# Optimization experiments

Hardware: AMD Instinct MI355X
Metric: run time of the kernel (lower is better)

## Reference

```python
import jax, jax.numpy as jnp
import numpy as np

E = 8           # num_experts
K = 2           # num_experts_per_tok
D = 1024        # hidden_size
F = 2048        # intermediate_dim
B, S = 1, 2048  # batch, seq_len


def setup_inputs() -> dict:
    key = jax.random.key(0)
    k0, k1, k2, k3, k4, k5 = jax.random.split(key, 6)
    hidden_states = jax.random.normal(k0, (B, S, D), dtype=jnp.float32)
    topk_weights = jax.random.uniform(k1, (B * S, K), dtype=jnp.float32)
    topk_ids = jax.random.randint(k2, (B * S, K), 0, E, dtype=jnp.int32)
    scale = 0.02
    wi_0 = jax.random.normal(k3, (E, D, F), dtype=jnp.float32) * scale
    wi_1 = jax.random.normal(k4, (E, D, F), dtype=jnp.float32) * scale
    wo = jax.random.normal(k5, (E, F, D), dtype=jnp.float32) * scale
    return {"hidden_states": hidden_states, "topk_weights": topk_weights,
            "topk_ids": topk_ids, "wi_0": wi_0, "wi_1": wi_1, "wo": wo}


def _gmm(x, w, group_sizes):
    """Grouped matmul: rows of x are sorted by expert; group_sizes[e] rows use w[e].
    Small fixed loop over experts (E=8); rows not owned by expert e are masked out."""
    n_e = w.shape[0]
    expert_of_row = jnp.repeat(jnp.arange(n_e), group_sizes,
                               total_repeat_length=x.shape[0])  # [M]
    out = jnp.zeros((x.shape[0], w.shape[2]), dtype=x.dtype)
    for e in range(n_e):
        out = out + jnp.where((expert_of_row == e)[:, None], x @ w[e], 0.0)
    return out


def _moe_forward(hidden_states, topk_weights, topk_ids, wi_0, wi_1, wo):
    b, s, d = hidden_states.shape
    k = topk_ids.shape[1]
    n_e = wi_0.shape[0]
    x2d = hidden_states.reshape(b * s, d)

    # ---- permute: sort expanded tokens by selected expert (stable) ----
    flat_experts = jnp.ravel(topk_ids)                       # [T*K]
    sort_idx = jnp.argsort(flat_experts, stable=True)        # [T*K]
    sorted_rows = sort_idx // k                              # source token per row
    x_sorted = jnp.take(x2d, sorted_rows, axis=0)            # [T*K, D]
    group_sizes = jnp.bincount(flat_experts, length=n_e)     # [E]

    # ---- grouped GEMMs with SwiGLU (gate * up, then down) ----
    g0 = _gmm(x_sorted, wi_0, group_sizes)                   # [T*K, F]
    g1 = _gmm(x_sorted, wi_1, group_sizes)                   # [T*K, F]
    h = jax.nn.silu(g0) * g1                                 # fused SiLU-gate
    y = _gmm(h, wo, group_sizes)                             # [T*K, D]

    # ---- unpermute and combine with routing weights (fp32 accum) ----
    unsort_idx = jnp.argsort(sort_idx, stable=True)
    y = jnp.take(y, unsort_idx, axis=0).reshape(b * s, k, d)
    out = jnp.einsum('bke,bk->be', y.astype(jnp.float32),
                     topk_weights.astype(jnp.float32))
    return out.reshape(b, s, d)


def reference(hidden_states, topk_weights, topk_ids, wi_0, wi_1, wo):
    return _moe_forward(hidden_states, topk_weights, topk_ids, wi_0, wi_1, wo)
```

## Files before the change

kernel.cpp:

```cpp
#include <hip/hip_runtime.h>
#include <hip/hip_bf16.h>


#define D_DIM 1024
#define F_DIM 2048
#define ROWS 4096
#define MAXTILE 40
#define LDK 72

using f32x4 = __attribute__((ext_vector_type(4))) float;
using s16x8 = __attribute__((ext_vector_type(8))) short;

__device__ __forceinline__ unsigned pack_trunc(float lo, float hi) {
  return (__float_as_uint(lo) >> 16) | (__float_as_uint(hi) & 0xffff0000u);
}
__device__ __forceinline__ unsigned short bf_rn(float f) {
  unsigned u = __float_as_uint(f);
  u += 0x7fffu + ((u >> 16) & 1u);
  return (unsigned short)(u >> 16);
}
__device__ __forceinline__ unsigned pack_rn(float lo, float hi) {
  return (unsigned)bf_rn(lo) | ((unsigned)bf_rn(hi) << 16);
}

typedef const __attribute__((address_space(1))) void* gp_t;
typedef __attribute__((address_space(3))) void* lp_t;
__device__ __forceinline__ void load16(const void* g, void* l) {
  __builtin_amdgcn_global_load_lds((gp_t)g, (lp_t)l, 16, 0, 0);
}

__global__ __launch_bounds__(512) void route_kernel(const int* __restrict__ ids,
                                                    int* __restrict__ sorted_flat,
                                                    int* __restrict__ unsort,
                                                    int* __restrict__ tile_meta) {
  __shared__ int cnt[8];
  __shared__ int off[9];
  const int tid = threadIdx.x;
  const int w = tid >> 6, lane = tid & 63;
  int c = 0;
  for (int base = 0; base < ROWS; base += 64) {
    int e = ids[base + lane];
    c += __popcll(__ballot(e == w));
  }
  if (lane == 0) cnt[w] = c;
  __syncthreads();
  if (tid == 0) {
    int o = 0;
    for (int e = 0; e < 8; e++) { off[e] = o; o += cnt[e]; }
    off[8] = o;
    int nT = 0;
    for (int e = 0; e < 8; e++) {
      for (int r0 = off[e]; r0 < off[e + 1]; r0 += 128) {
        tile_meta[1 + 3 * nT] = r0;
        tile_meta[2 + 3 * nT] = off[e + 1];
        tile_meta[3 + 3 * nT] = e;
        nT++;
      }
    }
    tile_meta[0] = nT;
  }
  __syncthreads();
  int pos = off[w];
  const unsigned long long below = (1ull << lane) - 1ull;
  for (int base = 0; base < ROWS; base += 64) {
    int e = ids[base + lane];
    unsigned long long m = __ballot(e == w);
    if (e == w) {
      int p = pos + __popcll(m & below);
      sorted_flat[p] = base + lane;
      unsort[base + lane] = p;
    }
    pos += __popcll(m);
  }
}

__global__ void zero_kernel(float4* __restrict__ p, int n4) {
  int i = blockIdx.x * blockDim.x + threadIdx.x;
  if (i < n4) p[i] = float4{0.f, 0.f, 0.f, 0.f};
}

__global__ __launch_bounds__(256) void convT_lds(
    const float* __restrict__ wi0, const float* __restrict__ wi1,
    const float* __restrict__ wo, unsigned short* __restrict__ w0T,
    unsigned short* __restrict__ w1T, unsigned short* __restrict__ woT) {
  __shared__ unsigned t[64 * 33];
  const int z = blockIdx.y;
  const int which = z >> 3, e = z & 7;
  const float* S;
  unsigned short* Dp;
  int Kd, Nd, nbits;
  if (which == 0)      { S = wi0; Dp = w0T; Kd = D_DIM; Nd = F_DIM; nbits = 5; }
  else if (which == 1) { S = wi1; Dp = w1T; Kd = D_DIM; Nd = F_DIM; nbits = 5; }
  else                 { S = wo;  Dp = woT; Kd = F_DIM; Nd = D_DIM; nbits = 4; }
  S  += (size_t)e * Kd * Nd;
  Dp += (size_t)e * Kd * Nd;
  const int n0 = (blockIdx.x & ((1 << nbits) - 1)) * 64;
  const int k0 = (blockIdx.x >> nbits) * 64;
  const int tid = threadIdx.x;
  const int nb = (tid & 15) * 4;
#pragma unroll
  for (int i = 0; i < 2; i++) {
    const int kp = (tid >> 4) + i * 16;
    const float* p = S + (size_t)(k0 + 2 * kp) * Nd + n0 + nb;
    float4 v0 = *(const float4*)p;
    float4 v1 = *(const float4*)(p + Nd);
    t[(nb + 0) * 33 + kp] = pack_rn(v0.x, v1.x);
    t[(nb + 1) * 33 + kp] = pack_rn(v0.y, v1.y);
    t[(nb + 2) * 33 + kp] = pack_rn(v0.z, v1.z);
    t[(nb + 3) * 33 + kp] = pack_rn(v0.w, v1.w);
  }
  __syncthreads();
  const int co = (tid & 7) * 4;
#pragma unroll
  for (int i = 0; i < 2; i++) {
    const int n = (tid >> 3) + i * 32;
    const unsigned* q = &t[n * 33 + co];
    uint4 o = make_uint4(q[0], q[1], q[2], q[3]);
    *(uint4*)(Dp + (size_t)(n0 + n) * Kd + k0 + co * 2) = o;
  }
}

__global__ __launch_bounds__(256) void gather_kernel(const float* __restrict__ x,
                                                     const int* __restrict__ sorted_flat,
                                                     unsigned short* __restrict__ xs) {
  const int r = blockIdx.x;
  const int tok = sorted_flat[r] >> 1;
  const float4 v = *(const float4*)(x + (size_t)tok * D_DIM + threadIdx.x * 4);
  *(uint2*)(xs + (size_t)r * D_DIM + threadIdx.x * 4) =
      make_uint2(pack_rn(v.x, v.y), pack_rn(v.z, v.w));
}

__device__ __forceinline__ int sw(int row, int chunk) {
  return row * 64 + ((chunk ^ (row & 7)) << 3);
}

__global__ __launch_bounds__(256, 2) void gemm1_kernel(
    const unsigned short* __restrict__ xs, const unsigned short* __restrict__ w0T,
    const unsigned short* __restrict__ w1T, const int* __restrict__ tile_meta,
    unsigned short* __restrict__ h) {
  __shared__ unsigned short As[128 * 64];
  __shared__ unsigned short B0s[128 * 64];
  __shared__ unsigned short B1s[128 * 64];
  const int tile = blockIdx.x;
  if (tile >= tile_meta[0]) return;
  const int row0 = tile_meta[1 + 3 * tile];
  const int rowEnd = tile_meta[2 + 3 * tile];
  const int e = tile_meta[3 + 3 * tile];
  const int n0 = blockIdx.y * 128;
  const unsigned short* W0 = w0T + ((size_t)e * F_DIM + n0) * D_DIM;
  const unsigned short* W1 = w1T + ((size_t)e * F_DIM + n0) * D_DIM;

  const int tid = threadIdx.x;
  const int lane = tid & 63, wv = tid >> 6;
  const int wm = (wv & 1) * 64, wn = (wv >> 1) * 64;
  const int lm = lane & 15, lq = lane >> 4;
  const int srow = lane >> 3;
  const int skk = ((lane & 7) ^ srow) << 3;

  f32x4 acc0[4][4], acc1[4][4];
#pragma unroll
  for (int i = 0; i < 4; i++)
#pragma unroll
    for (int j = 0; j < 4; j++) { acc0[i][j] = 0.f; acc1[i][j] = 0.f; }

  for (int k0 = 0; k0 < D_DIM; k0 += 64) {
    __syncthreads();
#pragma unroll
    for (int r = 0; r < 4; r++) {
      const int c = r * 4 + wv;
      const int m = c * 8 + srow;
      int mc = row0 + m; if (mc > ROWS - 1) mc = ROWS - 1;
      load16(xs + (size_t)mc * D_DIM + k0 + skk, (char*)As + c * 1024);
      load16(W0 + (size_t)m * D_DIM + k0 + skk, (char*)B0s + c * 1024);
      load16(W1 + (size_t)m * D_DIM + k0 + skk, (char*)B1s + c * 1024);
    }
    __syncthreads();
#pragma unroll
    for (int ks = 0; ks < 64; ks += 32) {
      const int cb = (ks >> 3) + lq;
      s16x8 af[4], b0[4], b1[4];
#pragma unroll
      for (int t = 0; t < 4; t++) {
        af[t] = *(const s16x8*)&As[sw(wm + t * 16 + lm, cb)];
        b0[t] = *(const s16x8*)&B0s[sw(wn + t * 16 + lm, cb)];
        b1[t] = *(const s16x8*)&B1s[sw(wn + t * 16 + lm, cb)];
      }
#pragma unroll
      for (int im = 0; im < 4; im++)
#pragma unroll
        for (int in = 0; in < 4; in++) {
          acc0[im][in] = __builtin_amdgcn_mfma_f32_16x16x32_bf16(
              af[im], b0[in], acc0[im][in], 0, 0, 0);
          acc1[im][in] = __builtin_amdgcn_mfma_f32_16x16x32_bf16(
              af[im], b1[in], acc1[im][in], 0, 0, 0);
        }
    }
  }
#pragma unroll
  for (int im = 0; im < 4; im++) {
    int gmB = row0 + wm + im * 16 + lq * 4;
#pragma unroll
    for (int in = 0; in < 4; in++) {
      int gn = n0 + wn + in * 16 + lm;
#pragma unroll
      for (int r = 0; r < 4; r++) {
        int gm = gmB + r;
        if (gm < rowEnd) {
          float g = acc0[im][in][r];
          float s = g / (1.f + __expf(-g));
          h[(size_t)gm * F_DIM + gn] = bf_rn(s * acc1[im][in][r]);
        }
      }
    }
  }
}

__global__ __launch_bounds__(256, 4) void gemm2_kernel(
    const unsigned short* __restrict__ h, const unsigned short* __restrict__ woT,
    const int* __restrict__ tile_meta, float* __restrict__ y) {
  __shared__ unsigned short As[128 * 64];
  __shared__ unsigned short Bs[64 * 64];
  const int tile = blockIdx.x;
  if (tile >= tile_meta[0]) return;
  const int row0 = tile_meta[1 + 3 * tile];
  const int rowEnd = tile_meta[2 + 3 * tile];
  const int e = tile_meta[3 + 3 * tile];
  const int n0 = blockIdx.y * 64;
  const unsigned short* W = woT + ((size_t)e * D_DIM + n0) * F_DIM;

  const int tid = threadIdx.x;
  const int lane = tid & 63, wv = tid >> 6;
  const int wm = (wv & 1) * 64, wn = (wv >> 1) * 32;
  const int lm = lane & 15, lq = lane >> 4;
  const int srow = lane >> 3;
  const int skk = ((lane & 7) ^ srow) << 3;

  f32x4 acc[4][2];
#pragma unroll
  for (int i = 0; i < 4; i++)
#pragma unroll
    for (int j = 0; j < 2; j++) acc[i][j] = 0.f;

  for (int k0 = 0; k0 < F_DIM; k0 += 64) {
    __syncthreads();
#pragma unroll
    for (int r = 0; r < 4; r++) {
      const int c = r * 4 + wv;
      const int m = c * 8 + srow;
      int mc = row0 + m; if (mc > ROWS - 1) mc = ROWS - 1;
      load16(h + (size_t)mc * F_DIM + k0 + skk, (char*)As + c * 1024);
    }
#pragma unroll
    for (int r = 0; r < 2; r++) {
      const int c = r * 4 + wv;
      const int m = c * 8 + srow;
      load16(W + (size_t)m * F_DIM + k0 + skk, (char*)Bs + c * 1024);
    }
    __syncthreads();
#pragma unroll
    for (int ks = 0; ks < 64; ks += 32) {
      const int cb = (ks >> 3) + lq;
      s16x8 af[4], bf[2];
#pragma unroll
      for (int t = 0; t < 4; t++)
        af[t] = *(const s16x8*)&As[sw(wm + t * 16 + lm, cb)];
#pragma unroll
      for (int t = 0; t < 2; t++)
        bf[t] = *(const s16x8*)&Bs[sw(wn + t * 16 + lm, cb)];
#pragma unroll
      for (int im = 0; im < 4; im++)
#pragma unroll
        for (int in = 0; in < 2; in++)
          acc[im][in] = __builtin_amdgcn_mfma_f32_16x16x32_bf16(
              af[im], bf[in], acc[im][in], 0, 0, 0);
    }
  }
#pragma unroll
  for (int im = 0; im < 4; im++) {
    int gmB = row0 + wm + im * 16 + lq * 4;
#pragma unroll
    for (int in = 0; in < 2; in++) {
      int gn = n0 + wn + in * 16 + lm;
#pragma unroll
      for (int r = 0; r < 4; r++) {
        int gm = gmB + r;
        if (gm < rowEnd) y[(size_t)gm * D_DIM + gn] = acc[im][in][r];
      }
    }
  }
}

__global__ __launch_bounds__(256) void combine_kernel(const float* __restrict__ y,
                                                      const float* __restrict__ tw,
                                                      const int* __restrict__ unsort,
                                                      float* __restrict__ out) {
  const int tkn = blockIdx.x;
  const int r0 = unsort[2 * tkn], r1 = unsort[2 * tkn + 1];
  const float w0 = tw[2 * tkn], w1 = tw[2 * tkn + 1];
  const int c = threadIdx.x * 4;
  float4 a = *(const float4*)(y + (size_t)r0 * D_DIM + c);
  float4 b = *(const float4*)(y + (size_t)r1 * D_DIM + c);
  float4 o = {w0 * a.x + w1 * b.x, w0 * a.y + w1 * b.y,
              w0 * a.z + w1 * b.z, w0 * a.w + w1 * b.w};
  *(float4*)(out + (size_t)tkn * D_DIM + c) = o;
}

__device__ __forceinline__ void stage_bt(const float* __restrict__ Wt, int ldw,
                                         unsigned short* Bs, int tid) {
#pragma unroll
  for (int it = 0; it < 4; it++) {
    const int kp = (tid & 7) + it * 8;
    const int nq = tid >> 3;
    const float* p = Wt + (size_t)(2 * kp) * ldw + nq * 4;
    const float4 va = *(const float4*)p;
    const float4 vb = *(const float4*)(p + ldw);
    unsigned short* b = Bs + (nq * 4) * LDK + 2 * kp;
    *(unsigned*)(b)           = pack_trunc(va.x, vb.x);
    *(unsigned*)(b + LDK)     = pack_trunc(va.y, vb.y);
    *(unsigned*)(b + 2 * LDK) = pack_trunc(va.z, vb.z);
    *(unsigned*)(b + 3 * LDK) = pack_trunc(va.w, vb.w);
  }
}

__global__ __launch_bounds__(256, 2) void gemm1_fb(
    const float* __restrict__ x, const float* __restrict__ wi0,
    const float* __restrict__ wi1, const int* __restrict__ sorted_flat,
    const int* __restrict__ tile_meta, unsigned short* __restrict__ h) {
  __shared__ unsigned short As[128 * LDK];
  __shared__ unsigned short B0s[128 * LDK];
  __shared__ unsigned short B1s[128 * LDK];
  __shared__ int tok[128];
  const int tile = blockIdx.x;
  if (tile >= tile_meta[0]) return;
  const int row0 = tile_meta[1 + 3 * tile];
  const int rowEnd = tile_meta[2 + 3 * tile];
  const int e = tile_meta[3 + 3 * tile];
  const int n0 = blockIdx.y * 128;
  const float* W0 = wi0 + (size_t)e * D_DIM * F_DIM;
  const float* W1 = wi1 + (size_t)e * D_DIM * F_DIM;
  const int tid = threadIdx.x;
  if (tid < 128) {
    int r = row0 + tid; if (r > ROWS - 1) r = ROWS - 1;
    tok[tid] = sorted_flat[r] >> 1;
  }
  f32x4 acc0[4][4], acc1[4][4];
#pragma unroll
  for (int i = 0; i < 4; i++)
#pragma unroll
    for (int j = 0; j < 4; j++) { acc0[i][j] = 0.f; acc1[i][j] = 0.f; }
  const int lane = tid & 63, wv = tid >> 6;
  const int wm = (wv & 1) * 64, wn = (wv >> 1) * 64;
  const int lm = lane & 15, lq = lane >> 4;
  for (int k0 = 0; k0 < D_DIM; k0 += 64) {
    __syncthreads();
#pragma unroll
    for (int i = 0; i < 8; i++) {
      int idx = tid + i * 256;
      int m = idx >> 4, kq = idx & 15;
      float4 v = *(const float4*)(x + (size_t)tok[m] * D_DIM + k0 + kq * 4);
      *(uint2*)&As[m * LDK + kq * 4] =
          make_uint2(pack_trunc(v.x, v.y), pack_trunc(v.z, v.w));
    }
    stage_bt(W0 + (size_t)k0 * F_DIM + n0, F_DIM, B0s, tid);
    stage_bt(W1 + (size_t)k0 * F_DIM + n0, F_DIM, B1s, tid);
    __syncthreads();
#pragma unroll
    for (int ks = 0; ks < 64; ks += 32) {
      s16x8 af[4], b0[4], b1[4];
#pragma unroll
      for (int t = 0; t < 4; t++) {
        af[t] = *(const s16x8*)&As[(wm + t * 16 + lm) * LDK + ks + lq * 8];
        b0[t] = *(const s16x8*)&B0s[(wn + t * 16 + lm) * LDK + ks + lq * 8];
        b1[t] = *(const s16x8*)&B1s[(wn + t * 16 + lm) * LDK + ks + lq * 8];
      }
#pragma unroll
      for (int im = 0; im < 4; im++)
#pragma unroll
        for (int in = 0; in < 4; in++) {
          acc0[im][in] = __builtin_amdgcn_mfma_f32_16x16x32_bf16(
              af[im], b0[in], acc0[im][in], 0, 0, 0);
          acc1[im][in] = __builtin_amdgcn_mfma_f32_16x16x32_bf16(
              af[im], b1[in], acc1[im][in], 0, 0, 0);
        }
    }
  }
#pragma unroll
  for (int im = 0; im < 4; im++) {
    int gmB = row0 + wm + im * 16 + lq * 4;
#pragma unroll
    for (int in = 0; in < 4; in++) {
      int gn = n0 + wn + in * 16 + lm;
#pragma unroll
      for (int r = 0; r < 4; r++) {
        int gm = gmB + r;
        if (gm < rowEnd) {
          float g = acc0[im][in][r];
          float s = g / (1.f + __expf(-g));
          h[(size_t)gm * F_DIM + gn] = bf_rn(s * acc1[im][in][r]);
        }
      }
    }
  }
}

__global__ __launch_bounds__(256, 3) void gemm2_fb(
    const unsigned short* __restrict__ h, const float* __restrict__ wo,
    const float* __restrict__ tw, const int* __restrict__ sorted_flat,
    const int* __restrict__ tile_meta, float* __restrict__ out) {
  __shared__ unsigned short As[128 * LDK];
  __shared__ unsigned short Bs[128 * LDK];
  __shared__ int sTok[128];
  __shared__ float sWgt[128];
  const int tile = blockIdx.x;
  if (tile >= tile_meta[0]) return;
  const int row0 = tile_meta[1 + 3 * tile];
  const int rowEnd = tile_meta[2 + 3 * tile];
  const int e = tile_meta[3 + 3 * tile];
  const int n0 = blockIdx.y * 128;
  const float* W = wo + (size_t)e * F_DIM * D_DIM;
  const int tid = threadIdx.x;
  if (tid < 128) {
    int r = row0 + tid; if (r > ROWS - 1) r = ROWS - 1;
    int fl = sorted_flat[r];
    sTok[tid] = fl >> 1;
    sWgt[tid] = tw[fl];
  }
  f32x4 acc[4][4];
#pragma unroll
  for (int i = 0; i < 4; i++)
#pragma unroll
    for (int j = 0; j < 4; j++) acc[i][j] = 0.f;
  const int lane = tid & 63, wv = tid >> 6;
  const int wm = (wv & 1) * 64, wn = (wv >> 1) * 64;
  const int lm = lane & 15, lq = lane >> 4;
  for (int k0 = 0; k0 < F_DIM; k0 += 64) {
    __syncthreads();
#pragma unroll
    for (int i = 0; i < 8; i++) {
      int idx = tid + i * 256;
      int m = idx >> 4, kq = idx & 15;
      int gm = row0 + m; if (gm > ROWS - 1) gm = ROWS - 1;
      *(uint2*)&As[m * LDK + kq * 4] =
          *(const uint2*)(h + (size_t)gm * F_DIM + k0 + kq * 4);
    }
    stage_bt(W + (size_t)k0 * D_DIM + n0, D_DIM, Bs, tid);
    __syncthreads();
#pragma unroll
    for (int ks = 0; ks < 64; ks += 32) {
      s16x8 af[4], bf[4];
#pragma unroll
      for (int t = 0; t < 4; t++) {
        af[t] = *(const s16x8*)&As[(wm + t * 16 + lm) * LDK + ks + lq * 8];
        bf[t] = *(const s16x8*)&Bs[(wn + t * 16 + lm) * LDK + ks + lq * 8];
      }
#pragma unroll
      for (int im = 0; im < 4; im++)
#pragma unroll
        for (int in = 0; in < 4; in++)
          acc[im][in] = __builtin_amdgcn_mfma_f32_16x16x32_bf16(
              af[im], bf[in], acc[im][in], 0, 0, 0);
    }
  }
#pragma unroll
  for (int im = 0; im < 4; im++) {
    int lrB = wm + im * 16 + lq * 4;
#pragma unroll
    for (int in = 0; in < 4; in++) {
      int gn = n0 + wn + in * 16 + lm;
#pragma unroll
      for (int r = 0; r < 4; r++) {
        int lr = lrB + r;
        int gm = row0 + lr;
        if (gm < rowEnd)
          atomicAdd(out + (size_t)sTok[lr] * D_DIM + gn, sWgt[lr] * acc[im][in][r]);
      }
    }
  }
}

extern "C" void kernel_launch(void* const* d_in, const int* in_sizes, int n_in,
                              void* d_out, int out_size, void* d_ws, size_t ws_size,
                              hipStream_t stream) {
  const float* x   = (const float*)d_in[0];
  const float* tw  = (const float*)d_in[1];
  const int*   ids = (const int*)d_in[2];
  const float* wi0 = (const float*)d_in[3];
  const float* wi1 = (const float*)d_in[4];
  const float* wo  = (const float*)d_in[5];
  float* out = (float*)d_out;

  int* tile_meta = (int*)d_ws;
  int* sorted_flat = tile_meta + 256;
  int* unsort = sorted_flat + ROWS;

  const size_t MB = 1024 * 1024;
  const size_t XS_OFF = 64 * 1024;
  const size_t H_OFF  = XS_OFF + 8 * MB;
  const size_t W0_OFF = H_OFF + 16 * MB;
  const size_t W1_OFF = W0_OFF + 32 * MB;
  const size_t WO_OFF = W1_OFF + 32 * MB;
  const size_t NEED   = WO_OFF + 32 * MB;

  route_kernel<<<1, 512, 0, stream>>>(ids, sorted_flat, unsort, tile_meta);
  if (ws_size >= NEED) {
    unsigned short* xs  = (unsigned short*)((char*)d_ws + XS_OFF);
    unsigned short* h   = (unsigned short*)((char*)d_ws + H_OFF);
    unsigned short* w0T = (unsigned short*)((char*)d_ws + W0_OFF);
    unsigned short* w1T = (unsigned short*)((char*)d_ws + W1_OFF);
    unsigned short* woT = (unsigned short*)((char*)d_ws + WO_OFF);
    float* y = (float*)((char*)d_ws + W0_OFF);

    convT_lds<<<dim3(512, 24), 256, 0, stream>>>(wi0, wi1, wo, w0T, w1T, woT);
    gather_kernel<<<ROWS, 256, 0, stream>>>(x, sorted_flat, xs);
    gemm1_kernel<<<dim3(MAXTILE, F_DIM / 128), 256, 0, stream>>>(xs, w0T, w1T,
                                                                 tile_meta, h);
    gemm2_kernel<<<dim3(MAXTILE, D_DIM / 64), 256, 0, stream>>>(h, woT,
                                                                tile_meta, y);
    combine_kernel<<<ROWS / 2, 256, 0, stream>>>(y, tw, unsort, out);
  } else {
    unsigned short* h = (unsigned short*)((char*)d_ws + XS_OFF);
    zero_kernel<<<(out_size / 4 + 255) / 256, 256, 0, stream>>>((float4*)out,
                                                                out_size / 4);
    gemm1_fb<<<dim3(MAXTILE, F_DIM / 128), 256, 0, stream>>>(x, wi0, wi1,
                                                             sorted_flat,
                                                             tile_meta, h);
    gemm2_fb<<<dim3(MAXTILE, D_DIM / 128), 256, 0, stream>>>(h, wo, tw,
                                                             sorted_flat,
                                                             tile_meta, out);
  }
}
```

Before: 342.5 us.

## Shrink gemm1 N-tile, enlarge convT K-tile, stage routing ids in LDS

gemm1 now uses 64-wide N tiles instead of 128. That halves the B tiles in LDS and the accumulator registers, doubles the grid and raises the occupancy hint to 3 blocks per CU. The weight transpose/convert kernel handles a 128-deep K slab per block, issuing all global loads before any LDS writes, and launches half as many blocks. The route kernel copies the ids into shared memory once instead of reading global memory twice. The smaller gemm1 tile lowers arithmetic intensity per A load, and the A tile is now reloaded twice as often.

```diff
diff --git a/kernel.cpp b/kernel.cpp
--- a/kernel.cpp
+++ b/kernel.cpp
@@ -33,15 +33,20 @@
                                                     int* __restrict__ sorted_flat,
                                                     int* __restrict__ unsort,
                                                     int* __restrict__ tile_meta) {
+  __shared__ int sid[ROWS];
   __shared__ int cnt[8];
   __shared__ int off[9];
   const int tid = threadIdx.x;
+#pragma unroll
+  for (int j = 0; j < 2; j++) {
+    int idx = tid + j * 512;
+    *(int4*)&sid[idx * 4] = *(const int4*)&ids[idx * 4];
+  }
+  __syncthreads();
   const int w = tid >> 6, lane = tid & 63;
   int c = 0;
-  for (int base = 0; base < ROWS; base += 64) {
-    int e = ids[base + lane];
-    c += __popcll(__ballot(e == w));
-  }
+  for (int base = 0; base < ROWS; base += 64)
+    c += __popcll(__ballot(sid[base + lane] == w));
   if (lane == 0) cnt[w] = c;
   __syncthreads();
   if (tid == 0) {
@@ -63,9 +68,8 @@
   int pos = off[w];
   const unsigned long long below = (1ull << lane) - 1ull;
   for (int base = 0; base < ROWS; base += 64) {
-    int e = ids[base + lane];
-    unsigned long long m = __ballot(e == w);
-    if (e == w) {
+    unsigned long long m = __ballot(sid[base + lane] == w);
+    if (sid[base + lane] == w) {
       int p = pos + __popcll(m & below);
       sorted_flat[p] = base + lane;
       unsort[base + lane] = p;
@@ -83,7 +87,7 @@
     const float* __restrict__ wi0, const float* __restrict__ wi1,
     const float* __restrict__ wo, unsigned short* __restrict__ w0T,
     unsigned short* __restrict__ w1T, unsigned short* __restrict__ woT) {
-  __shared__ unsigned t[64 * 33];
+  __shared__ unsigned t[64 * 65];
   const int z = blockIdx.y;
   const int which = z >> 3, e = z & 7;
   const float* S;
@@ -95,28 +99,33 @@
   S  += (size_t)e * Kd * Nd;
   Dp += (size_t)e * Kd * Nd;
   const int n0 = (blockIdx.x & ((1 << nbits) - 1)) * 64;
-  const int k0 = (blockIdx.x >> nbits) * 64;
+  const int k0 = (blockIdx.x >> nbits) * 128;
   const int tid = threadIdx.x;
   const int nb = (tid & 15) * 4;
-#pragma unroll
-  for (int i = 0; i < 2; i++) {
+  float4 v[4][2];
+#pragma unroll
+  for (int i = 0; i < 4; i++) {
     const int kp = (tid >> 4) + i * 16;
     const float* p = S + (size_t)(k0 + 2 * kp) * Nd + n0 + nb;
-    float4 v0 = *(const float4*)p;
-    float4 v1 = *(const float4*)(p + Nd);
-    t[(nb + 0) * 33 + kp] = pack_rn(v0.x, v1.x);
-    t[(nb + 1) * 33 + kp] = pack_rn(v0.y, v1.y);
-    t[(nb + 2) * 33 + kp] = pack_rn(v0.z, v1.z);
-    t[(nb + 3) * 33 + kp] = pack_rn(v0.w, v1.w);
+    v[i][0] = *(const float4*)p;
+    v[i][1] = *(const float4*)(p + Nd);
+  }
+#pragma unroll
+  for (int i = 0; i < 4; i++) {
+    const int kp = (tid >> 4) + i * 16;
+    t[(nb + 0) * 65 + kp] = pack_rn(v[i][0].x, v[i][1].x);
+    t[(nb + 1) * 65 + kp] = pack_rn(v[i][0].y, v[i][1].y);
+    t[(nb + 2) * 65 + kp] = pack_rn(v[i][0].z, v[i][1].z);
+    t[(nb + 3) * 65 + kp] = pack_rn(v[i][0].w, v[i][1].w);
   }
   __syncthreads();
-  const int co = (tid & 7) * 4;
-#pragma unroll
-  for (int i = 0; i < 2; i++) {
-    const int n = (tid >> 3) + i * 32;
-    const unsigned* q = &t[n * 33 + co];
+  const int c = tid & 15;
+#pragma unroll
+  for (int j = 0; j < 4; j++) {
+    const int n = (tid >> 4) + j * 16;
+    const unsigned* q = &t[n * 65 + c * 4];
     uint4 o = make_uint4(q[0], q[1], q[2], q[3]);
-    *(uint4*)(Dp + (size_t)(n0 + n) * Kd + k0 + co * 2) = o;
+    *(uint4*)(Dp + (size_t)(n0 + n) * Kd + k0 + c * 8) = o;
   }
 }
 
@@ -134,34 +143,34 @@
   return row * 64 + ((chunk ^ (row & 7)) << 3);
 }
 
-__global__ __launch_bounds__(256, 2) void gemm1_kernel(
+__global__ __launch_bounds__(256, 3) void gemm1_kernel(
     const unsigned short* __restrict__ xs, const unsigned short* __restrict__ w0T,
     const unsigned short* __restrict__ w1T, const int* __restrict__ tile_meta,
     unsigned short* __restrict__ h) {
   __shared__ unsigned short As[128 * 64];
-  __shared__ unsigned short B0s[128 * 64];
-  __shared__ unsigned short B1s[128 * 64];
+  __shared__ unsigned short B0s[64 * 64];
+  __shared__ unsigned short B1s[64 * 64];
   const int tile = blockIdx.x;
   if (tile >= tile_meta[0]) return;
   const int row0 = tile_meta[1 + 3 * tile];
   const int rowEnd = tile_meta[2 + 3 * tile];
   const int e = tile_meta[3 + 3 * tile];
-  const int n0 = blockIdx.y * 128;
+  const int n0 = blockIdx.y * 64;
   const unsigned short* W0 = w0T + ((size_t)e * F_DIM + n0) * D_DIM;
   const unsigned short* W1 = w1T + ((size_t)e * F_DIM + n0) * D_DIM;
 
   const int tid = threadIdx.x;
   const int lane = tid & 63, wv = tid >> 6;
-  const int wm = (wv & 1) * 64, wn = (wv >> 1) * 64;
+  const int wm = (wv & 1) * 64, wn = (wv >> 1) * 32;
   const int lm = lane & 15, lq = lane >> 4;
   const int srow = lane >> 3;
   const int skk = ((lane & 7) ^ srow) << 3;
 
-  f32x4 acc0[4][4], acc1[4][4];
+  f32x4 acc0[4][2], acc1[4][2];
 #pragma unroll
   for (int i = 0; i < 4; i++)
 #pragma unroll
-    for (int j = 0; j < 4; j++) { acc0[i][j] = 0.f; acc1[i][j] = 0.f; }
+    for (int j = 0; j < 2; j++) { acc0[i][j] = 0.f; acc1[i][j] = 0.f; }
 
   for (int k0 = 0; k0 < D_DIM; k0 += 64) {
     __syncthreads();
@@ -171,6 +180,11 @@
       const int m = c * 8 + srow;
       int mc = row0 + m; if (mc > ROWS - 1) mc = ROWS - 1;
       load16(xs + (size_t)mc * D_DIM + k0 + skk, (char*)As + c * 1024);
+    }
+#pragma unroll
+    for (int r = 0; r < 2; r++) {
+      const int c = r * 4 + wv;
+      const int m = c * 8 + srow;
       load16(W0 + (size_t)m * D_DIM + k0 + skk, (char*)B0s + c * 1024);
       load16(W1 + (size_t)m * D_DIM + k0 + skk, (char*)B1s + c * 1024);
     }
@@ -178,17 +192,19 @@
 #pragma unroll
     for (int ks = 0; ks < 64; ks += 32) {
       const int cb = (ks >> 3) + lq;
-      s16x8 af[4], b0[4], b1[4];
-#pragma unroll
-      for (int t = 0; t < 4; t++) {
+      s16x8 af[4], b0[2], b1[2];
+#pragma unroll
+      for (int t = 0; t < 4; t++)
         af[t] = *(const s16x8*)&As[sw(wm + t * 16 + lm, cb)];
+#pragma unroll
+      for (int t = 0; t < 2; t++) {
         b0[t] = *(const s16x8*)&B0s[sw(wn + t * 16 + lm, cb)];
         b1[t] = *(const s16x8*)&B1s[sw(wn + t * 16 + lm, cb)];
       }
 #pragma unroll
       for (int im = 0; im < 4; im++)
 #pragma unroll
-        for (int in = 0; in < 4; in++) {
+        for (int in = 0; in < 2; in++) {
           acc0[im][in] = __builtin_amdgcn_mfma_f32_16x16x32_bf16(
               af[im], b0[in], acc0[im][in], 0, 0, 0);
           acc1[im][in] = __builtin_amdgcn_mfma_f32_16x16x32_bf16(
@@ -200,7 +216,7 @@
   for (int im = 0; im < 4; im++) {
     int gmB = row0 + wm + im * 16 + lq * 4;
 #pragma unroll
-    for (int in = 0; in < 4; in++) {
+    for (int in = 0; in < 2; in++) {
       int gn = n0 + wn + in * 16 + lm;
 #pragma unroll
       for (int r = 0; r < 4; r++) {
@@ -510,10 +526,10 @@
     unsigned short* woT = (unsigned short*)((char*)d_ws + WO_OFF);
     float* y = (float*)((char*)d_ws + W0_OFF);
 
-    convT_lds<<<dim3(512, 24), 256, 0, stream>>>(wi0, wi1, wo, w0T, w1T, woT);
+    convT_lds<<<dim3(256, 24), 256, 0, stream>>>(wi0, wi1, wo, w0T, w1T, woT);
     gather_kernel<<<ROWS, 256, 0, stream>>>(x, sorted_flat, xs);
-    gemm1_kernel<<<dim3(MAXTILE, F_DIM / 128), 256, 0, stream>>>(xs, w0T, w1T,
-                                                                 tile_meta, h);
+    gemm1_kernel<<<dim3(MAXTILE, F_DIM / 64), 256, 0, stream>>>(xs, w0T, w1T,
+                                                                tile_meta, h);
     gemm2_kernel<<<dim3(MAXTILE, D_DIM / 64), 256, 0, stream>>>(h, woT,
                                                                 tile_meta, y);
     combine_kernel<<<ROWS / 2, 256, 0, stream>>>(y, tw, unsort, out);
```

After: 324.5 us. -5.2%, faster.
